# Kernel optimization log

Measured on AMD Instinct MI355X. Metric: run time of the kernel, lower is better.

## Reference

```python
import jax, jax.numpy as jnp
import numpy as np

B, T, D = 1, 2048, 1024
H, HD, NH = 16, 64, 2        # heads, head_dim, num_householder
EPS = 1e-5                   # RMSNorm eps
SCALE = HD ** -0.5           # query scale (k_dim**-0.5)


def setup_inputs() -> dict:
    key = jax.random.key(0)
    ks = jax.random.split(key, 10)
    init = lambda k, shape: jax.random.normal(k, shape, jnp.float32) * (shape[0] ** -0.5)
    return {
        "x": jax.random.normal(ks[0], (B, T, D), jnp.float32),
        "Wq": init(ks[1], (D, H * HD)),
        "Wk": init(ks[2], (D, NH * H * HD)),
        "Wv": init(ks[3], (D, NH * H * HD)),
        "Wb": init(ks[4], (D, NH * H)),
        "Wa": init(ks[5], (D, H)),
        "A_log": jnp.log(jax.random.uniform(ks[6], (H,), jnp.float32, 1e-2, 16.0)),
        "dt_bias": jnp.zeros((H,), jnp.float32),
        "Wg": init(ks[7], (D, H * HD)),
        "norm_weight": jnp.ones((HD,), jnp.float32),
        "Wo": init(ks[8], (H * HD, D)),
    }


def _l2norm(t):
    return t * jax.lax.rsqrt(jnp.sum(t * t, -1, keepdims=True) + 1e-6)


def _forward(x, Wq, Wk, Wv, Wb, Wa, A_log, dt_bias, Wg, norm_weight, Wo):
    # projections; householder sub-steps interleaved along time -> length T*NH
    q = _l2norm((x @ Wq).reshape(B, T, H, HD)) * SCALE            # [B,T,H,HD]
    k = _l2norm((x @ Wk).reshape(B, T, NH, H, HD)).reshape(B, T * NH, H, HD)
    v = (x @ Wv).reshape(B, T * NH, H, HD)
    # allow_neg_eigval=True -> beta in (0,2)
    beta = 2.0 * jax.nn.sigmoid((x @ Wb).reshape(B, T * NH, H))
    # gated decay applied once per token (first sub-step), zeros for the rest
    g = -jnp.exp(A_log) * jax.nn.softplus(x @ Wa + dt_bias)       # [B,T,H]
    g = jnp.concatenate(
        [g[:, :, None], jnp.zeros((B, T, NH - 1, H), g.dtype)], axis=2
    ).reshape(B, T * NH, H)
    qf = jnp.repeat(q, NH, axis=1)  # only sub-step NH-1 outputs are kept

    def step(S, inp):
        # S: [B,H,HD_k,HD_v] recurrent state
        k_t, v_t, b_t, g_t, q_t = inp
        S = S * jnp.exp(g_t)[..., None, None]
        pred = jnp.einsum('bhk,bhkv->bhv', k_t, S)
        dv = (v_t - pred) * b_t[..., None]
        S = S + k_t[..., None] * dv[..., None, :]
        o = jnp.einsum('bhk,bhkv->bhv', q_t, S)
        return S, o

    tm = lambda a: jnp.swapaxes(a, 0, 1)  # time-major for scan
    S0 = jnp.zeros((B, H, HD, HD), x.dtype)
    _, o = jax.lax.scan(step, S0, (tm(k), tm(v), tm(beta), tm(g), tm(qf)))
    o = tm(o[NH - 1::NH])  # last householder sub-step per token -> [B,T,H,HD]

    # gated RMSNorm (FusedRMSNormGated with swish gate)
    o = o * jax.lax.rsqrt(jnp.mean(o * o, -1, keepdims=True) + EPS) * norm_weight
    gate = (x @ Wg).reshape(B, T, H, HD)
    o = o * (gate * jax.nn.sigmoid(gate))
    return o.reshape(B, T, H * HD) @ Wo


def reference(x, Wq, Wk, Wv, Wb, Wa, A_log, dt_bias, Wg, norm_weight, Wo):
    return _forward(x, Wq, Wk, Wv, Wb, Wa, A_log, dt_bias, Wg, norm_weight, Wo)
```

## Files before the change

### kernel.cpp

```cpp
#include <hip/hip_runtime.h>
#include <stdint.h>


typedef unsigned short u16;
typedef __attribute__((ext_vector_type(8))) short bf16x8;
typedef __attribute__((ext_vector_type(4))) float f32x4;
typedef __attribute__((ext_vector_type(2))) float f32x2;
typedef __attribute__((ext_vector_type(4))) unsigned short u16x4;

#define TT 2048
#define NP 6208
#define NC 64
#define CS 64

__device__ __forceinline__ u16 f2bf(float f) {
  union { float f; uint32_t u; } v; v.f = f;
  uint32_t r = v.u + 0x7fffu + ((v.u >> 16) & 1u);
  return (u16)(r >> 16);
}
__device__ __forceinline__ float bf2f(u16 b) {
  union { uint32_t u; float f; } v; v.u = ((uint32_t)b) << 16; return v.f;
}

__device__ __forceinline__ void gload_lds16(const u16* g, u16* l) {
  __builtin_amdgcn_global_load_lds(
      (__attribute__((address_space(1))) const void*)(uintptr_t)g,
      (__attribute__((address_space(3))) void*)(uint32_t)(uintptr_t)l, 16, 0, 0);
}

__global__ void cvt_kernel(const float* __restrict__ src, u16* __restrict__ dst, long n) {
  long i = (long)blockIdx.x * 256 + threadIdx.x;
  if (i < n) dst[i] = f2bf(src[i]);
}

__global__ __launch_bounds__(256) void transAll_kernel(
    const float* __restrict__ Wq, const float* __restrict__ Wk,
    const float* __restrict__ Wv, const float* __restrict__ Wb,
    const float* __restrict__ Wa, const float* __restrict__ Wg,
    const float* __restrict__ Wo, u16* __restrict__ WT, u16* __restrict__ WoT) {
  int bx = blockIdx.x;
  const float* src; u16* dst; int cols;
  if      (bx < 32)  { src = Wq; dst = WT;                cols = 1024; }
  else if (bx < 96)  { src = Wk; dst = WT + 1024UL*1024;  cols = 2048; bx -= 32; }
  else if (bx < 160) { src = Wv; dst = WT + 3072UL*1024;  cols = 2048; bx -= 96; }
  else if (bx < 161) { src = Wb; dst = WT + 5120UL*1024;  cols = 32;   bx -= 160; }
  else if (bx < 162) { src = Wa; dst = WT + 5152UL*1024;  cols = 16;   bx -= 161; }
  else if (bx < 194) { src = Wg; dst = WT + 5168UL*1024;  cols = 1024; bx -= 162; }
  else               { src = Wo; dst = WoT;               cols = 1024; bx -= 194; }
  __shared__ float tile[32][33];
  const int tx = threadIdx.x & 31, ty = threadIdx.x >> 5;
  const int c0 = bx * 32, r0 = blockIdx.y * 32;
  for (int rr = ty; rr < 32; rr += 8)
    if (c0 + tx < cols) tile[rr][tx] = src[(size_t)(r0 + rr) * cols + c0 + tx];
  __syncthreads();
  for (int rr = ty; rr < 32; rr += 8)
    if (c0 + rr < cols) dst[(size_t)(c0 + rr) * 1024 + r0 + tx] = f2bf(tile[tx][rr]);
}

__global__ __launch_bounds__(256) void beacon_kernel(float* __restrict__ out, int n) {
  int i = blockIdx.x * 256 + threadIdx.x;
  if (i < n) out[i] = 4000.0f;
}

__global__ __launch_bounds__(256) void gemm128(const u16* __restrict__ A,
    const u16* __restrict__ BT, float* __restrict__ Cf, u16* __restrict__ Cb,
    int K, int lda, int ldc, int Nmax, int out_bf16) {
  const int bm = blockIdx.x * 128, bn = blockIdx.y * 128;
  const int tid = threadIdx.x, w = tid >> 6, lane = tid & 63;
  const int wr = (w >> 1) * 64, wc = (w & 1) * 64;
  const int quad = lane >> 4, r = lane & 15;
  __shared__ u16 As[128][32], Bs[128][32];
  f32x4 acc[4][4] = {};
  const int sr = w * 32 + (lane >> 2);
  const int sc = (lane & 3) * 8;
  const u16* gA0 = A  + (size_t)(bm + sr) * lda + sc;
  const u16* gA1 = A  + (size_t)(bm + sr + 16) * lda + sc;
  const u16* gB0 = BT + (size_t)(bn + sr) * K + sc;
  const u16* gB1 = BT + (size_t)(bn + sr + 16) * K + sc;
  u16* lA0 = &As[w * 32][0];
  u16* lA1 = &As[w * 32 + 16][0];
  u16* lB0 = &Bs[w * 32][0];
  u16* lB1 = &Bs[w * 32 + 16][0];
  for (int ks = 0; ks < K; ks += 32) {
    __syncthreads();
    gload_lds16(gA0 + ks, lA0);
    gload_lds16(gA1 + ks, lA1);
    gload_lds16(gB0 + ks, lB0);
    gload_lds16(gB1 + ks, lB1);
    __syncthreads();
    bf16x8 af[4], bf[4];
#pragma unroll
    for (int i = 0; i < 4; i++) af[i] = *(const bf16x8*)&As[wr + i * 16 + r][quad * 8];
#pragma unroll
    for (int j = 0; j < 4; j++) bf[j] = *(const bf16x8*)&Bs[wc + j * 16 + r][quad * 8];
#pragma unroll
    for (int i = 0; i < 4; i++)
#pragma unroll
      for (int j = 0; j < 4; j++)
        acc[i][j] = __builtin_amdgcn_mfma_f32_16x16x32_bf16(af[i], bf[j], acc[i][j], 0, 0, 0);
  }
#pragma unroll
  for (int i = 0; i < 4; i++)
#pragma unroll
    for (int j = 0; j < 4; j++)
#pragma unroll
      for (int rg = 0; rg < 4; rg++) {
        int row = bm + wr + i * 16 + quad * 4 + rg;
        int col = bn + wc + j * 16 + r;
        if (col < Nmax) {
          float v = acc[i][j][rg];
          if (out_bf16) Cb[(size_t)row * ldc + col] = f2bf(v);
          else          Cf[(size_t)row * ldc + col] = v;
        }
      }
}

__global__ __launch_bounds__(64) void prep_kernel(float* __restrict__ P,
    const float* __restrict__ A_log, const float* __restrict__ dt_bias,
    float* __restrict__ betab, float* __restrict__ gbuf) {
  const int t = blockIdx.x >> 4, h = blockIdx.x & 15, lane = threadIdx.x;
  float* Pt = P + (size_t)t * NP;
  float qv = Pt[h * 64 + lane];
  float ss = qv * qv;
#pragma unroll
  for (int off = 32; off; off >>= 1) ss += __shfl_xor(ss, off);
  Pt[h * 64 + lane] = qv * rsqrtf(ss + 1e-6f) * 0.125f;
#pragma unroll
  for (int nh = 0; nh < 2; nh++) {
    float kv = Pt[1024 + nh * 1024 + h * 64 + lane];
    float ks = kv * kv;
#pragma unroll
    for (int off = 32; off; off >>= 1) ks += __shfl_xor(ks, off);
    Pt[1024 + nh * 1024 + h * 64 + lane] = kv * rsqrtf(ks + 1e-6f);
  }
  if (lane < 2) {
    float bb = Pt[5120 + lane * 16 + h];
    betab[(size_t)(2 * t + lane) * 16 + h] = 2.f / (1.f + expf(-bb));
  }
  if (lane == 0) {
    float a = Pt[5152 + h] + dt_bias[h];
    float sp = (a > 20.f) ? a : log1pf(expf(a));
    gbuf[t * 16 + h] = -expf(A_log[h]) * sp;
  }
}

__global__ __launch_bounds__(256, 1) void phaseA_kernel(const float* __restrict__ P,
    const float* __restrict__ betab, const float* __restrict__ gbuf,
    u16* __restrict__ Wbuf, u16* __restrict__ Uvbuf,
    float* __restrict__ Mbuf, float* __restrict__ NTbuf, float* __restrict__ cumbuf) {
  const int c = blockIdx.x, h = blockIdx.y, tid = threadIdx.x;
  const int bi = tid >> 4, bj = tid & 15;
  __shared__ float LA[64][68];
  __shared__ float LB[64][68];
  __shared__ float LC[64][68];
  __shared__ float cumch[64], betach[64], bbch[64], rowfl[64];
  const size_t base = ((size_t)c * 16 + h) * 4096;

  for (int e = tid; e < 4096; e += 256) {
    int i = e >> 6, d = e & 63, s = c * 64 + i, t = s >> 1, nh = s & 1;
    float kv = P[(size_t)t * NP + 1024 + nh * 1024 + h * 64 + d];
    LB[i][d] = kv; LA[d][i] = kv;
  }
  if (tid < 64) betach[tid] = betab[(size_t)(c * 64 + tid) * 16 + h];
  __syncthreads();
  if (tid == 0) {
    float cum = 0.f;
    for (int i = 0; i < 64; i++) {
      if ((i & 1) == 0) cum += gbuf[(c * 32 + (i >> 1)) * 16 + h];
      cumch[i] = cum;
    }
  }
  __syncthreads();
  if (tid < 64) {
    bbch[tid] = betach[tid] * expf(cumch[tid]);
    rowfl[tid] = expf(cumch[63] - cumch[tid]);
  }
  {
    float acc[4][4] = {};
#pragma unroll 4
    for (int d = 0; d < 64; d++) {
      f32x4 a = *(const f32x4*)&LA[d][4 * bi];
      f32x4 b = *(const f32x4*)&LA[d][4 * bj];
#pragma unroll
      for (int rr = 0; rr < 4; rr++)
#pragma unroll
        for (int cc = 0; cc < 4; cc++) acc[rr][cc] += a[rr] * b[cc];
    }
#pragma unroll
    for (int rr = 0; rr < 4; rr++)
#pragma unroll
      for (int cc = 0; cc < 4; cc++) {
        int i = 4 * bi + rr, j = 4 * bj + cc;
        LC[i][j] = (j < i) ? betach[i] * expf(cumch[i] - cumch[j]) * acc[rr][cc] : 0.f;
      }
  }
  __syncthreads();
  {
    int col = tid >> 2, part = tid & 3;
    if (part == 0) LA[col][0] = (col == 0) ? 1.f : 0.f;
    for (int i = 1; i < 64; i++) {
      float partial = 0.f;
      for (int j = col + part; j < i; j += 4) partial += LC[i][j] * LA[col][j];
      partial += __shfl_xor(partial, 1);
      partial += __shfl_xor(partial, 2);
      if (part == 0) LA[col][i] = ((i == col) ? 1.f : 0.f) - partial;
    }
  }
  __syncthreads();
  float vreg[16];
  {
    const int vi = tid >> 6, vd = tid & 63;
#pragma unroll
    for (int s = 0; s < 16; s++) {
      int i = vi + 4 * s, ss = c * 64 + i, t = ss >> 1, nh = ss & 1;
      vreg[s] = P[(size_t)t * NP + 3072 + nh * 1024 + h * 64 + vd];
    }
  }
  {
    float acc[4][4] = {};
#pragma unroll 4
    for (int j = 0; j < 4 * bi + 4; j++) {
      f32x4 tv = *(const f32x4*)&LA[j][4 * bi];
      f32x4 kv = *(const f32x4*)&LB[j][4 * bj];
      float bbj = bbch[j];
#pragma unroll
      for (int rr = 0; rr < 4; rr++)
#pragma unroll
        for (int cc = 0; cc < 4; cc++) acc[rr][cc] += tv[rr] * bbj * kv[cc];
    }
#pragma unroll
    for (int rr = 0; rr < 4; rr++) {
      int i = 4 * bi + rr;
      u16x4 wb;
#pragma unroll
      for (int cc = 0; cc < 4; cc++) { LC[i][4 * bj + cc] = acc[rr][cc]; wb[cc] = f2bf(acc[rr][cc]); }
      *(u16x4*)&Wbuf[base + (size_t)i * 64 + 4 * bj] = wb;
    }
  }
  __syncthreads();
  {
    const float bL = expf(cumch[63]);
    float acc[4][4] = {};
#pragma unroll 4
    for (int i = 0; i < 64; i++) {
      f32x4 kv = *(const f32x4*)&LB[i][4 * bi];
      f32x4 wv = *(const f32x4*)&LC[i][4 * bj];
      float rf = rowfl[i];
#pragma unroll
      for (int rr = 0; rr < 4; rr++)
#pragma unroll
        for (int cc = 0; cc < 4; cc++) acc[rr][cc] += rf * kv[rr] * wv[cc];
    }
#pragma unroll
    for (int rr = 0; rr < 4; rr++) {
      int m = 4 * bi + rr;
      f32x4 mv;
#pragma unroll
      for (int cc = 0; cc < 4; cc++)
        mv[cc] = ((m == 4 * bj + cc) ? bL : 0.f) - acc[rr][cc];
      *(f32x4*)&Mbuf[base + (size_t)m * 64 + 4 * bj] = mv;
    }
  }
  __syncthreads();
  {
    const int vi = tid >> 6, vd = tid & 63;
#pragma unroll
    for (int s = 0; s < 16; s++) LC[vi + 4 * s][vd] = vreg[s];
  }
  __syncthreads();
  float ua[4][4] = {};
  {
#pragma unroll 4
    for (int j = 0; j < 4 * bi + 4; j++) {
      f32x4 tv = *(const f32x4*)&LA[j][4 * bi];
      f32x4 vv = *(const f32x4*)&LC[j][4 * bj];
      float be = betach[j];
#pragma unroll
      for (int rr = 0; rr < 4; rr++)
#pragma unroll
        for (int cc = 0; cc < 4; cc++) ua[rr][cc] += tv[rr] * be * vv[cc];
    }
  }
  __syncthreads();
  {
#pragma unroll
    for (int rr = 0; rr < 4; rr++) {
      int i = 4 * bi + rr;
      u16x4 ub;
#pragma unroll
      for (int cc = 0; cc < 4; cc++) { LA[i][4 * bj + cc] = ua[rr][cc]; ub[cc] = f2bf(ua[rr][cc]); }
      *(u16x4*)&Uvbuf[base + (size_t)i * 64 + 4 * bj] = ub;
    }
  }
  __syncthreads();
  {
    float acc[4][4] = {};
#pragma unroll 4
    for (int i = 0; i < 64; i++) {
      f32x4 kv = *(const f32x4*)&LB[i][4 * bi];
      f32x4 uv = *(const f32x4*)&LA[i][4 * bj];
      float rf = rowfl[i];
#pragma unroll
      for (int rr = 0; rr < 4; rr++)
#pragma unroll
        for (int cc = 0; cc < 4; cc++) acc[rr][cc] += rf * kv[rr] * uv[cc];
    }
#pragma unroll
    for (int cc = 0; cc < 4; cc++) {
      f32x4 nv;
#pragma unroll
      for (int rr = 0; rr < 4; rr++) nv[rr] = acc[rr][cc];
      *(f32x4*)&NTbuf[base + (size_t)(4 * bj + cc) * 64 + 4 * bi] = nv;
    }
  }
  if (tid < 64) cumbuf[((size_t)c * 16 + h) * 64 + tid] = cumch[tid];
}

__global__ __launch_bounds__(64) void phaseB_kernel(const float* __restrict__ Mbuf,
    const float* __restrict__ NTbuf, u16* __restrict__ S0Tbuf) {
  const int g = blockIdx.x, h = blockIdx.y, l = threadIdx.x;
  const int c0 = 2 * g, c1 = 2 * g + 1;
  __shared__ float Ssh[2][2][64];
  Ssh[0][0][l] = 0.f; Ssh[0][1][l] = 0.f;
  float s0 = 0.f, s1 = 0.f;
  f32x4 mreg[16];
  float n0, n1;
  {
    const float* Mc = Mbuf + (size_t)h * 4096 + (size_t)l * 64;
#pragma unroll
    for (int q = 0; q < 16; q++) mreg[q] = *(const f32x4*)(Mc + 4 * q);
    const float* Nc = NTbuf + (size_t)h * 4096;
    n0 = Nc[c0 * 64 + l]; n1 = Nc[c1 * 64 + l];
  }
  __syncthreads();
  int p = 0;
  for (int c = 0; c < NC; c++) {
    const size_t base = ((size_t)c * 16 + h) * 4096;
    S0Tbuf[base + (size_t)c0 * 64 + l] = f2bf(s0);
    S0Tbuf[base + (size_t)c1 * 64 + l] = f2bf(s1);
    f32x4 mnext[16]; float nn0 = 0.f, nn1 = 0.f;
    if (c + 1 < NC) {
      const float* Mn = Mbuf + ((size_t)(c + 1) * 16 + h) * 4096 + (size_t)l * 64;
#pragma unroll
      for (int q = 0; q < 16; q++) mnext[q] = *(const f32x4*)(Mn + 4 * q);
      const float* Nn = NTbuf + ((size_t)(c + 1) * 16 + h) * 4096;
      nn0 = Nn[c0 * 64 + l]; nn1 = Nn[c1 * 64 + l];
    }
    float acc0 = n0, acc1 = n1;
#pragma unroll
    for (int q = 0; q < 16; q++) {
      f32x4 mv = mreg[q];
      f32x4 sv0 = *(const f32x4*)&Ssh[p][0][4 * q];
      f32x4 sv1 = *(const f32x4*)&Ssh[p][1][4 * q];
#pragma unroll
      for (int t = 0; t < 4; t++) { acc0 += mv[t] * sv0[t]; acc1 += mv[t] * sv1[t]; }
    }
    s0 = acc0; s1 = acc1;
    Ssh[p ^ 1][0][l] = s0; Ssh[p ^ 1][1][l] = s1;
    __syncthreads();
    p ^= 1;
#pragma unroll
    for (int q = 0; q < 16; q++) mreg[q] = mnext[q];
    n0 = nn0; n1 = nn1;
  }
}

__global__ __launch_bounds__(256) void phaseB2_kernel(const u16* __restrict__ Wbuf,
    const u16* __restrict__ S0Tbuf, u16* __restrict__ Uvbuf) {
  const int c = blockIdx.x, h = blockIdx.y, tid = threadIdx.x;
  const int bi = tid >> 4, bd = tid & 15;
  __shared__ float WTl[64][68], S0l[64][68];
  const size_t base = ((size_t)c * 16 + h) * 4096;
  for (int e = tid; e < 4096; e += 256) {
    int i = e >> 6, m = e & 63;
    WTl[m][i] = bf2f(Wbuf[base + e]);
    S0l[m][i] = bf2f(S0Tbuf[base + e]);
  }
  __syncthreads();
  float acc[4][4] = {};
#pragma unroll 4
  for (int m = 0; m < 64; m++) {
    f32x4 wv = *(const f32x4*)&WTl[m][4 * bi];
    f32x4 sv = *(const f32x4*)&S0l[m][4 * bd];
#pragma unroll
    for (int rr = 0; rr < 4; rr++)
#pragma unroll
      for (int cc = 0; cc < 4; cc++) acc[rr][cc] += wv[rr] * sv[cc];
  }
#pragma unroll
  for (int rr = 0; rr < 4; rr++) {
    int i = 4 * bi + rr;
    u16x4 uv = *(const u16x4*)&Uvbuf[base + (size_t)i * 64 + 4 * bd];
    u16x4 ob;
#pragma unroll
    for (int cc = 0; cc < 4; cc++) ob[cc] = f2bf(bf2f(uv[cc]) - acc[rr][cc]);
    *(u16x4*)&Uvbuf[base + (size_t)i * 64 + 4 * bd] = ob;
  }
}

__global__ __launch_bounds__(256) void phaseC_kernel(const float* __restrict__ P,
    const float* __restrict__ cumbuf, const u16* __restrict__ Ubuf,
    const u16* __restrict__ S0Tbuf, const float* __restrict__ nw,
    u16* __restrict__ ybuf) {
  const int c = blockIdx.x, h = blockIdx.y, tid = threadIdx.x;
  const int rb = tid >> 4, jb = tid & 15;
  __shared__ float qT[64][36];
  __shared__ float kTc[64][68];
  __shared__ float Ul[64][68];
  __shared__ float PmT[64][36];
  __shared__ float cuml[64], nwl[64];
  const size_t base = (size_t)c * 16 + h;
  for (int e = tid; e < 2048; e += 256) {
    int r = e >> 6, d = e & 63;
    qT[d][r] = P[(size_t)(c * 32 + r) * NP + h * 64 + d];
  }
  for (int e = tid; e < 4096; e += 256) {
    int j = e >> 6, d = e & 63, s = c * 64 + j, t = s >> 1, nh = s & 1;
    kTc[d][j] = P[(size_t)t * NP + 1024 + nh * 1024 + h * 64 + d];
    Ul[j][d] = bf2f(Ubuf[base * 4096 + e]);
  }
  if (tid < 64) { cuml[tid] = cumbuf[base * 64 + tid]; nwl[tid] = nw[tid]; }
  __syncthreads();
  {
    float pa[2][4] = {};
#pragma unroll 4
    for (int d = 0; d < 64; d++) {
      f32x2 qv = *(const f32x2*)&qT[d][2 * rb];
      f32x4 kv = *(const f32x4*)&kTc[d][4 * jb];
#pragma unroll
      for (int rr = 0; rr < 2; rr++)
#pragma unroll
        for (int cc = 0; cc < 4; cc++) pa[rr][cc] += qv[rr] * kv[cc];
    }
#pragma unroll
    for (int rr = 0; rr < 2; rr++)
#pragma unroll
      for (int cc = 0; cc < 4; cc++) {
        int r = 2 * rb + rr, i = 2 * r + 1, j = 4 * jb + cc;
        PmT[j][r] = (j <= i) ? expf(cuml[i] - cuml[j]) * pa[rr][cc] : 0.f;
      }
  }
  __syncthreads();
  for (int e = tid; e < 4096; e += 256) {
    int d = e >> 6, m = e & 63;
    kTc[m][d] = bf2f(S0Tbuf[base * 4096 + e]);
  }
  __syncthreads();
  float o[2][4];
  {
    float a1[2][4] = {}, a2[2][4] = {};
#pragma unroll 4
    for (int m = 0; m < 64; m++) {
      f32x2 qv = *(const f32x2*)&qT[m][2 * rb];
      f32x4 sv = *(const f32x4*)&kTc[m][4 * jb];
#pragma unroll
      for (int rr = 0; rr < 2; rr++)
#pragma unroll
        for (int cc = 0; cc < 4; cc++) a1[rr][cc] += qv[rr] * sv[cc];
    }
#pragma unroll 4
    for (int j = 0; j < 4 * rb + 4; j++) {
      f32x2 pv = *(const f32x2*)&PmT[j][2 * rb];
      f32x4 uv = *(const f32x4*)&Ul[j][4 * jb];
#pragma unroll
      for (int rr = 0; rr < 2; rr++)
#pragma unroll
        for (int cc = 0; cc < 4; cc++) a2[rr][cc] += pv[rr] * uv[cc];
    }
#pragma unroll
    for (int rr = 0; rr < 2; rr++) {
      float ec = expf(cuml[2 * (2 * rb + rr) + 1]);
#pragma unroll
      for (int cc = 0; cc < 4; cc++) o[rr][cc] = a1[rr][cc] * ec + a2[rr][cc];
    }
  }
  __syncthreads();
  float* ol = &qT[0][0];
#pragma unroll
  for (int rr = 0; rr < 2; rr++)
#pragma unroll
    for (int cc = 0; cc < 4; cc++)
      ol[(2 * rb + rr) * 68 + 4 * jb + cc] = o[rr][cc];
  __syncthreads();
  for (int e = tid; e < 2048; e += 256) {
    int r = e >> 6, d = e & 63;
    float ov = ol[r * 68 + d];
    float ss = ov * ov;
#pragma unroll
    for (int off = 32; off; off >>= 1) ss += __shfl_xor(ss, off);
    float on = ov * rsqrtf(ss * (1.f / 64.f) + 1e-5f) * nwl[d];
    int t = c * 32 + r;
    float gt = P[(size_t)t * NP + 5168 + h * 64 + d];
    float sw = gt / (1.f + expf(-gt));
    ybuf[(size_t)t * 1024 + h * 64 + d] = f2bf(on * sw);
  }
}

extern "C" void kernel_launch(void* const* d_in, const int* in_sizes, int n_in,
                              void* d_out, int out_size, void* d_ws, size_t ws_size,
                              hipStream_t stream) {
  const float* x       = (const float*)d_in[0];
  const float* Wq      = (const float*)d_in[1];
  const float* Wk      = (const float*)d_in[2];
  const float* Wv      = (const float*)d_in[3];
  const float* Wb      = (const float*)d_in[4];
  const float* Wa      = (const float*)d_in[5];
  const float* A_log   = (const float*)d_in[6];
  const float* dt_bias = (const float*)d_in[7];
  const float* Wg      = (const float*)d_in[8];
  const float* nw      = (const float*)d_in[9];
  const float* Wo      = (const float*)d_in[10];
  float* out = (float*)d_out;

  char* w = (char*)d_ws;
  size_t used = 0;
  auto alloc = [&](size_t bytes) {
    char* p = w + used; used += (bytes + 255) & ~(size_t)255; return p;
  };
  u16*   xb    = (u16*)  alloc(2048UL * 1024 * 2);
  u16*   WT    = (u16*)  alloc(6272UL * 1024 * 2);
  u16*   WoT   = (u16*)  alloc(1024UL * 1024 * 2);
  float* P     = (float*)alloc(2048UL * NP * 4);
  float* betab = (float*)alloc(4096UL * 16 * 4);
  float* gbuf  = (float*)alloc(2048UL * 16 * 4);
  u16*   ybuf  = (u16*)  alloc(2048UL * 1024 * 2);
  u16*   Wbuf  = (u16*)  alloc((size_t)NC * 16 * 4096 * 2);
  u16*   Uvbuf = (u16*)  alloc((size_t)NC * 16 * 4096 * 2);
  u16*   S0Tb  = (u16*)  alloc((size_t)NC * 16 * 4096 * 2);
  float* Mbuf  = (float*)alloc((size_t)NC * 16 * 4096 * 4);
  float* NTbuf = (float*)alloc((size_t)NC * 16 * 4096 * 4);
  float* cumb  = (float*)alloc((size_t)NC * 16 * 64 * 4);

  auto tgrid = [](long n) { return dim3((unsigned)((n + 255) / 256)); };
  if (used > ws_size) {
    beacon_kernel<<<tgrid(out_size), 256, 0, stream>>>(out, out_size);
    return;
  }

  hipMemsetAsync(WT + 6192UL * 1024, 0, 80UL * 1024 * 2, stream);

  cvt_kernel<<<tgrid(2048L*1024), 256, 0, stream>>>(x, xb, 2048L * 1024);
  transAll_kernel<<<dim3(226, 32), 256, 0, stream>>>(Wq, Wk, Wv, Wb, Wa, Wg, Wo, WT, WoT);

  gemm128<<<dim3(16, 49), 256, 0, stream>>>(xb, WT, P, nullptr, 1024, 1024, NP, NP, 0);
  prep_kernel<<<dim3(2048 * 16), 64, 0, stream>>>(P, A_log, dt_bias, betab, gbuf);

  phaseA_kernel<<<dim3(NC, 16), 256, 0, stream>>>(P, betab, gbuf, Wbuf, Uvbuf, Mbuf, NTbuf, cumb);
  phaseB_kernel<<<dim3(32, 16), 64, 0, stream>>>(Mbuf, NTbuf, S0Tb);
  phaseB2_kernel<<<dim3(NC, 16), 256, 0, stream>>>(Wbuf, S0Tb, Uvbuf);
  phaseC_kernel<<<dim3(NC, 16), 256, 0, stream>>>(P, cumb, Uvbuf, S0Tb, nw, ybuf);

  gemm128<<<dim3(16, 8), 256, 0, stream>>>(ybuf, WoT, out, nullptr, 1024, 1024, 1024, 1024, 0);
}
```

Before: 427.4 us.

## Fuse W/U and M/N chunk matmuls in phaseA and shorten triangular solve

In the chunk-preparation kernel, the W and U products now run in one loop over the inverted triangular matrix, sharing its loads, and the M and N products run in a second fused loop, so several barriers and LDS passes disappear. The forward-substitution solve keeps the two most recent solution entries in registers, and the V loads are issued before the solve so their latency can overlap it. The g decay values are staged into shared memory, which removes one barrier. In exchange the kernel holds two accumulator tiles at once, which raises register pressure.

```diff
diff --git a/kernel.cpp b/kernel.cpp
--- a/kernel.cpp
+++ b/kernel.cpp
@@ -154,19 +154,20 @@
   __shared__ float LB[64][68];
   __shared__ float LC[64][68];
   __shared__ float cumch[64], betach[64], bbch[64], rowfl[64];
+  __shared__ float gtmp[32];
   const size_t base = ((size_t)c * 16 + h) * 4096;
 
+  if (tid < 32) gtmp[tid] = gbuf[(c * 32 + tid) * 16 + h];
   for (int e = tid; e < 4096; e += 256) {
     int i = e >> 6, d = e & 63, s = c * 64 + i, t = s >> 1, nh = s & 1;
     float kv = P[(size_t)t * NP + 1024 + nh * 1024 + h * 64 + d];
     LB[i][d] = kv; LA[d][i] = kv;
   }
   if (tid < 64) betach[tid] = betab[(size_t)(c * 64 + tid) * 16 + h];
-  __syncthreads();
   if (tid == 0) {
     float cum = 0.f;
     for (int i = 0; i < 64; i++) {
-      if ((i & 1) == 0) cum += gbuf[(c * 32 + (i >> 1)) * 16 + h];
+      if ((i & 1) == 0) cum += gtmp[i >> 1];
       cumch[i] = cum;
     }
   }
@@ -195,18 +196,6 @@
       }
   }
   __syncthreads();
-  {
-    int col = tid >> 2, part = tid & 3;
-    if (part == 0) LA[col][0] = (col == 0) ? 1.f : 0.f;
-    for (int i = 1; i < 64; i++) {
-      float partial = 0.f;
-      for (int j = col + part; j < i; j += 4) partial += LC[i][j] * LA[col][j];
-      partial += __shfl_xor(partial, 1);
-      partial += __shfl_xor(partial, 2);
-      if (part == 0) LA[col][i] = ((i == col) ? 1.f : 0.f) - partial;
-    }
-  }
-  __syncthreads();
   float vreg[16];
   {
     const int vi = tid >> 6, vd = tid & 63;
@@ -217,39 +206,86 @@
     }
   }
   {
-    float acc[4][4] = {};
+    const int col = tid >> 2, part = tid & 3;
+    if (part == 0) LA[col][0] = (col == 0) ? 1.f : 0.f;
+    float tp1 = (col == 0) ? 1.f : 0.f;
+    float tp2 = 0.f;
+    for (int i = 1; i < 64; i++) {
+      float partial = 0.f;
+      for (int j = col + part; j < i - 2; j += 4)
+        partial += LC[i][j] * LA[col][j];
+      if (i >= 2 && (i - 2) >= col && ((i - 2 - col) & 3) == part)
+        partial += LC[i][i - 2] * tp2;
+      if ((i - 1) >= col && ((i - 1 - col) & 3) == part)
+        partial += LC[i][i - 1] * tp1;
+      partial += __shfl_xor(partial, 1);
+      partial += __shfl_xor(partial, 2);
+      float tn = ((i == col) ? 1.f : 0.f) - partial;
+      if (part == 0) LA[col][i] = tn;
+      tp2 = tp1; tp1 = tn;
+    }
+  }
+  __syncthreads();
+  {
+    const int vi = tid >> 6, vd = tid & 63;
+#pragma unroll
+    for (int s = 0; s < 16; s++) LC[vi + 4 * s][vd] = vreg[s];
+  }
+  __syncthreads();
+  float wacc[4][4] = {}, uacc[4][4] = {};
+  {
 #pragma unroll 4
     for (int j = 0; j < 4 * bi + 4; j++) {
       f32x4 tv = *(const f32x4*)&LA[j][4 * bi];
       f32x4 kv = *(const f32x4*)&LB[j][4 * bj];
+      f32x4 vv = *(const f32x4*)&LC[j][4 * bj];
       float bbj = bbch[j];
+      float bej = betach[j];
 #pragma unroll
       for (int rr = 0; rr < 4; rr++)
 #pragma unroll
-        for (int cc = 0; cc < 4; cc++) acc[rr][cc] += tv[rr] * bbj * kv[cc];
+        for (int cc = 0; cc < 4; cc++) {
+          wacc[rr][cc] += tv[rr] * bbj * kv[cc];
+          uacc[rr][cc] += tv[rr] * bej * vv[cc];
+        }
     }
 #pragma unroll
     for (int rr = 0; rr < 4; rr++) {
       int i = 4 * bi + rr;
-      u16x4 wb;
-#pragma unroll
-      for (int cc = 0; cc < 4; cc++) { LC[i][4 * bj + cc] = acc[rr][cc]; wb[cc] = f2bf(acc[rr][cc]); }
+      u16x4 wb, ub;
+#pragma unroll
+      for (int cc = 0; cc < 4; cc++) { wb[cc] = f2bf(wacc[rr][cc]); ub[cc] = f2bf(uacc[rr][cc]); }
       *(u16x4*)&Wbuf[base + (size_t)i * 64 + 4 * bj] = wb;
+      *(u16x4*)&Uvbuf[base + (size_t)i * 64 + 4 * bj] = ub;
+    }
+  }
+  __syncthreads();
+#pragma unroll
+  for (int rr = 0; rr < 4; rr++) {
+    int i = 4 * bi + rr;
+#pragma unroll
+    for (int cc = 0; cc < 4; cc++) {
+      LC[i][4 * bj + cc] = wacc[rr][cc];
+      LA[i][4 * bj + cc] = uacc[rr][cc];
     }
   }
   __syncthreads();
   {
     const float bL = expf(cumch[63]);
-    float acc[4][4] = {};
+    float macc[4][4] = {}, nacc[4][4] = {};
 #pragma unroll 4
     for (int i = 0; i < 64; i++) {
       f32x4 kv = *(const f32x4*)&LB[i][4 * bi];
       f32x4 wv = *(const f32x4*)&LC[i][4 * bj];
+      f32x4 uv = *(const f32x4*)&LA[i][4 * bj];
       float rf = rowfl[i];
 #pragma unroll
       for (int rr = 0; rr < 4; rr++)
 #pragma unroll
-        for (int cc = 0; cc < 4; cc++) acc[rr][cc] += rf * kv[rr] * wv[cc];
+        for (int cc = 0; cc < 4; cc++) {
+          macc[rr][cc] += rf * kv[rr] * wv[cc];
+          nacc[rr][cc] += rf * kv[rr] * uv[cc];
+        }
     }
 #pragma unroll
     for (int rr = 0; rr < 4; rr++) {
@@ -257,59 +293,14 @@
       f32x4 mv;
 #pragma unroll
       for (int cc = 0; cc < 4; cc++)
-        mv[cc] = ((m == 4 * bj + cc) ? bL : 0.f) - acc[rr][cc];
+        mv[cc] = ((m == 4 * bj + cc) ? bL : 0.f) - macc[rr][cc];
       *(f32x4*)&Mbuf[base + (size_t)m * 64 + 4 * bj] = mv;
-    }
-  }
-  __syncthreads();
-  {
-    const int vi = tid >> 6, vd = tid & 63;
-#pragma unroll
-    for (int s = 0; s < 16; s++) LC[vi + 4 * s][vd] = vreg[s];
-  }
-  __syncthreads();
-  float ua[4][4] = {};
-  {
-#pragma unroll 4
-    for (int j = 0; j < 4 * bi + 4; j++) {
-      f32x4 tv = *(const f32x4*)&LA[j][4 * bi];
-      f32x4 vv = *(const f32x4*)&LC[j][4 * bj];
-      float be = betach[j];
-#pragma unroll
-      for (int rr = 0; rr < 4; rr++)
-#pragma unroll
-        for (int cc = 0; cc < 4; cc++) ua[rr][cc] += tv[rr] * be * vv[cc];
-    }
-  }
-  __syncthreads();
-  {
-#pragma unroll
-    for (int rr = 0; rr < 4; rr++) {
-      int i = 4 * bi + rr;
-      u16x4 ub;
-#pragma unroll
-      for (int cc = 0; cc < 4; cc++) { LA[i][4 * bj + cc] = ua[rr][cc]; ub[cc] = f2bf(ua[rr][cc]); }
-      *(u16x4*)&Uvbuf[base + (size_t)i * 64 + 4 * bj] = ub;
-    }
-  }
-  __syncthreads();
-  {
-    float acc[4][4] = {};
-#pragma unroll 4
-    for (int i = 0; i < 64; i++) {
-      f32x4 kv = *(const f32x4*)&LB[i][4 * bi];
-      f32x4 uv = *(const f32x4*)&LA[i][4 * bj];
-      float rf = rowfl[i];
-#pragma unroll
-      for (int rr = 0; rr < 4; rr++)
-#pragma unroll
-        for (int cc = 0; cc < 4; cc++) acc[rr][cc] += rf * kv[rr] * uv[cc];
     }
 #pragma unroll
     for (int cc = 0; cc < 4; cc++) {
       f32x4 nv;
 #pragma unroll
-      for (int rr = 0; rr < 4; rr++) nv[rr] = acc[rr][cc];
+      for (int rr = 0; rr < 4; rr++) nv[rr] = nacc[rr][cc];
       *(f32x4*)&NTbuf[base + (size_t)(4 * bj + cc) * 64 + 4 * bi] = nv;
     }
   }
```

Result: slower. 446.6 us (+4.5%).
